# Performance work log

Measured on AMD Instinct MI355X. Metric: run time of the kernel, lower is better.

The kernel has to match this reference:

```python
import jax, jax.numpy as jnp
import numpy as np
from jax import lax

N = 16384
K = 16
EPS = 1e-5


def setup_inputs() -> dict:
    key = jax.random.key(0)
    ks = jax.random.split(key, 10)

    def w(k, shape):
        fan_in = shape[0]
        return jax.random.normal(k, shape, jnp.float32) / np.sqrt(fan_in)

    return {
        "pos": jax.random.normal(ks[0], (N, 3), jnp.float32),
        "normal": jax.random.normal(ks[1], (N, 3), jnp.float32),
        # conv1 mlp: Linear(9,64) -> GroupNorm(8,64) -> ReLU -> Linear(64,64)
        "W1a": w(ks[2], (9, 64)), "b1a": jnp.zeros((64,), jnp.float32),
        "g1": jnp.ones((64,), jnp.float32), "beta1": jnp.zeros((64,), jnp.float32),
        "W1b": w(ks[3], (64, 64)), "b1b": jnp.zeros((64,), jnp.float32),
        # conv2 mlp: Linear(67,64) -> GroupNorm(8,64) -> ReLU -> Linear(64,64)
        "W2a": w(ks[4], (67, 64)), "b2a": jnp.zeros((64,), jnp.float32),
        "g2": jnp.ones((64,), jnp.float32), "beta2": jnp.zeros((64,), jnp.float32),
        "W2b": w(ks[5], (64, 64)), "b2b": jnp.zeros((64,), jnp.float32),
        # conv3 mlp: Linear(67,128) -> GroupNorm(16,128) -> ReLU -> Linear(128,128)
        "W3a": w(ks[6], (67, 128)), "b3a": jnp.zeros((128,), jnp.float32),
        "g3": jnp.ones((128,), jnp.float32), "beta3": jnp.zeros((128,), jnp.float32),
        "W3b": w(ks[7], (128, 128)), "b3b": jnp.zeros((128,), jnp.float32),
    }


def knn_graph(pos, k):
    # [N,N] squared distances; loop=True -> self is included (distance 0).
    sq = jnp.sum(pos * pos, axis=1)
    d2 = sq[:, None] + sq[None, :] - 2.0 * (pos @ pos.T)
    _, nbr = lax.top_k(-d2, k)  # [N,k] neighbor (source) indices per target node
    return nbr


def group_norm(h, gamma, beta, groups):
    # h: [N,k,C]; normalize each group of channels per edge sample.
    n, k, c = h.shape
    hg = h.reshape(n, k, groups, c // groups)
    mu = hg.mean(axis=-1, keepdims=True)
    var = hg.var(axis=-1, keepdims=True)
    hg = (hg - mu) * lax.rsqrt(var + EPS)
    return hg.reshape(n, k, c) * gamma + beta


def pointnet_conv(x, pos, nbr, Wa, ba, gamma, beta, Wb, bb, groups):
    # message: concat(x_j, pos_j - pos_i), MLP per edge, max-aggregate over neighbors
    xj = x[nbr]                              # [N,k,C_in]
    rel = pos[nbr] - pos[:, None, :]         # [N,k,3]
    m = jnp.concatenate([xj, rel], axis=-1)  # [N,k,C_in+3]
    h = m @ Wa + ba
    h = jax.nn.relu(group_norm(h, gamma, beta, groups))
    h = h @ Wb + bb
    return jnp.max(h, axis=1)                # [N,C_out]


def reference(pos, normal, W1a, b1a, g1, beta1, W1b, b1b,
              W2a, b2a, g2, beta2, W2b, b2b,
              W3a, b3a, g3, beta3, W3b, b3b):
    nbr = knn_graph(pos, K)
    h = jnp.concatenate([pos, normal], axis=-1)  # [N,6]
    h1 = jax.nn.relu(pointnet_conv(h, pos, nbr, W1a, b1a, g1, beta1, W1b, b1b, 8))
    h2 = jax.nn.relu(pointnet_conv(h1, pos, nbr, W2a, b2a, g2, beta2, W2b, b2b, 8))
    h3 = jax.nn.relu(pointnet_conv(h2, pos, nbr, W3a, b3a, g3, beta3, W3b, b3b, 16))
    return (h1, h2, h3)
```

## Files before the change

### kernel.cpp

```cpp
#include <hip/hip_runtime.h>
#include <hip/hip_bf16.h>
#include <stdint.h>

typedef unsigned long long u64;
typedef unsigned int u32;
typedef __attribute__((ext_vector_type(8))) short bf16x8;
typedef __attribute__((ext_vector_type(4))) float f32x4;

__device__ __forceinline__ float ldv(const void* p, size_t idx, int mode) {
  return mode ? __bfloat162float(((const __hip_bfloat16*)p)[idx])
              : ((const float*)p)[idx];
}
__device__ __forceinline__ void stv(void* p, size_t idx, int mode, float v) {
  if (mode) ((__hip_bfloat16*)p)[idx] = __float2bfloat16(v);
  else      ((float*)p)[idx] = v;
}
__device__ __forceinline__ unsigned short f2bfb(float f) {
  u32 u = __float_as_uint(f);
  u32 r = u + 0x7fffu + ((u >> 16) & 1u);
  return (unsigned short)(r >> 16);
}
__device__ __forceinline__ u64 shfl64(u64 v, int src) {
  int lo = __shfl((int)(u32)(v & 0xffffffffu), src, 64);
  int hi = __shfl((int)(u32)(v >> 32), src, 64);
  return ((u64)(u32)hi << 32) | (u32)lo;
}
__device__ __forceinline__ u64 shfl_up64(u64 v, int d) {
  int lo = __shfl_up((int)(u32)(v & 0xffffffffu), d, 64);
  int hi = __shfl_up((int)(u32)(v >> 32), d, 64);
  return ((u64)(u32)hi << 32) | (u32)lo;
}

__global__ void PointNetSimple_61409442398998_kernel() {}

__global__ void detect_kernel(const void* __restrict__ pos, int* __restrict__ flag) {
  if (threadIdx.x == 0 && blockIdx.x == 0) {
    const unsigned short* u = (const unsigned short*)pos;
    int cnt = 0;
    for (int k = 0; k < 32; ++k) {
      int e = (u[k] >> 7) & 0xff;
      if (e >= 110 && e <= 140) cnt++;
    }
    flag[0] = (cnt >= 26) ? 1 : 0;
  }
}

struct CvtEnt { const void* src; float* dst; int n; };
struct CvtArgs { CvtEnt e[12]; };
__global__ void cvt_kernel(CvtArgs a, const int* __restrict__ flag) {
  const int mode = flag[0];
  CvtEnt ent = a.e[blockIdx.x];
  for (int t = threadIdx.x; t < ent.n; t += blockDim.x)
    ent.dst[t] = ldv(ent.src, t, mode);
}

struct WEnt { const void* src; unsigned short* dst; int K, N, Kpad; };
struct WArgs { WEnt e[6]; };
__global__ void wcvt_kernel(WArgs a, const int* __restrict__ flag) {
  const int mode = flag[0];
  WEnt ent = a.e[blockIdx.x];
  for (int t = threadIdx.x; t < ent.N * ent.Kpad; t += blockDim.x) {
    int nn = t / ent.Kpad;
    int k  = t - nn * ent.Kpad;
    float v = (k < ent.K) ? ldv(ent.src, (size_t)k * ent.N + nn, mode) : 0.0f;
    ent.dst[t] = f2bfb(v);
  }
}

__global__ void prep_kernel(const void* __restrict__ pos,
                            const void* __restrict__ nrm,
                            const int* __restrict__ flag,
                            float4* __restrict__ pos4,
                            float* __restrict__ h0, int n) {
  const int mode = flag[0];
  int i = blockIdx.x * blockDim.x + threadIdx.x;
  if (i >= n) return;
  float x = ldv(pos, 3*(size_t)i+0, mode);
  float y = ldv(pos, 3*(size_t)i+1, mode);
  float z = ldv(pos, 3*(size_t)i+2, mode);
  pos4[i] = make_float4(x, y, z, x*x + y*y + z*z);
  h0[6*(size_t)i+0] = x; h0[6*(size_t)i+1] = y; h0[6*(size_t)i+2] = z;
  h0[6*(size_t)i+3] = ldv(nrm, 3*(size_t)i+0, mode);
  h0[6*(size_t)i+4] = ldv(nrm, 3*(size_t)i+1, mode);
  h0[6*(size_t)i+5] = ldv(nrm, 3*(size_t)i+2, mode);
}

#define KNN_TPB 512
#define KNN_WPB 8
#define KCH 1024

__device__ __forceinline__ void knn_process(u64 bal, float d2, int base,
                                            u64& val, u64& t15, float& th,
                                            int lane) {
  while (bal) {
    int src = __ffsll((long long)bal) - 1;
    bal &= bal - 1;
    float ds = __shfl(d2, src, 64);
    u64 key = ((u64)__float_as_uint(ds) << 32) | (u32)(base + src);
    if (key < t15) {
      u64 prev = shfl_up64(val, 1);
      if (lane == 0) prev = 0ull;
      val = (key < prev) ? prev : ((key < val) ? key : val);
      t15 = shfl64(val, 15);
      th = __uint_as_float((u32)(t15 >> 32));
    }
  }
}

__global__ __launch_bounds__(KNN_TPB) void knn3_kernel(
    const float4* __restrict__ pos4, int* __restrict__ nbr, int n) {
  __shared__ float4 sp[2][KCH];
  const int tid  = threadIdx.x;
  const int lane = tid & 63;
  const int wid  = tid >> 6;
  const int i    = blockIdx.x * KNN_WPB + wid;
  const float4 pi = pos4[i];

  u64 val = ~0ull;
  u64 t15 = ~0ull;
  float th = __uint_as_float(0xffffffffu);
  th = 1e38f;

  for (int t = tid; t < KCH; t += KNN_TPB) sp[0][t] = pos4[t];
  __syncthreads();

  const int nch = n / KCH;
  for (int c = 0; c < nch; ++c) {
    const int cur = c & 1;
    float4 pre0, pre1;
    const bool more = (c + 1 < nch);
    if (more) {
      pre0 = pos4[(size_t)(c+1)*KCH + tid];
      pre1 = pos4[(size_t)(c+1)*KCH + KNN_TPB + tid];
    }
#pragma unroll 2
    for (int t = 0; t < KCH; t += 128) {
      float4 a = sp[cur][t + lane];
      float4 b = sp[cur][t + 64 + lane];
      float da = (pi.w + a.w) - 2.0f*(pi.x*a.x + pi.y*a.y + pi.z*a.z);
      float db = (pi.w + b.w) - 2.0f*(pi.x*b.x + pi.y*b.y + pi.z*b.z);
      da = fmaxf(da, 0.0f); db = fmaxf(db, 0.0f);
      int base = c*KCH + t;
      u64 bal = __ballot(da <= th);
      if (bal) knn_process(bal, da, base, val, t15, th, lane);
      bal = __ballot(db <= th);
      if (bal) knn_process(bal, db, base + 64, val, t15, th, lane);
    }
    if (more) {
      sp[cur^1][tid] = pre0;
      sp[cur^1][KNN_TPB + tid] = pre1;
    }
    __syncthreads();
  }
  if (lane < 16) nbr[(size_t)i*16 + lane] = (int)(val & 0xffffffffu);
}

template<int CIN, int CMID, int KT1, int NT, int KT2>
__global__ __launch_bounds__(256) void conv_mfma2_kernel(
    const float* __restrict__ xin,
    const float4* __restrict__ pos4,
    const int* __restrict__ nbr,
    const int* __restrict__ flag,
    const unsigned short* __restrict__ WaT,
    const unsigned short* __restrict__ WbT,
    const float* __restrict__ baf,
    const float* __restrict__ gmf,
    const float* __restrict__ btf,
    const float* __restrict__ bbf,
    float* __restrict__ xout,
    void* __restrict__ bout, size_t out_off)
{
  constexpr int K1PAD = KT1 * 32;
  constexpr int SB = CMID + 8;

  __shared__ unsigned short msgB[128 * SB];
  __shared__ float stage[4][32][20];

  const int tid  = threadIdx.x;
  const int lane = tid & 63;
  const int w    = tid >> 6;
  const int quad = lane >> 4;
  const int cl   = lane & 15;
  const int node0 = blockIdx.x * 8;
  const int mode = flag[0];

  bf16x8 afr[2][KT1];
#pragma unroll
  for (int mt = 0; mt < 2; ++mt) {
    const int node = node0 + w*2 + mt;
    const int j = nbr[(size_t)node*16 + cl];
    const float4 pin = pos4[node];
    const float4 pj = pos4[j];
    const float rx = pj.x - pin.x, ry = pj.y - pin.y, rz = pj.z - pin.z;
    if constexpr (CIN == 64) {
#pragma unroll
      for (int kt = 0; kt < 2; ++kt) {
        const float* p = &xin[(size_t)j*64 + kt*32 + quad*8];
        float4 a = *(const float4*)p;
        float4 b = *(const float4*)(p + 4);
        unsigned short o[8] = {f2bfb(a.x), f2bfb(a.y), f2bfb(a.z), f2bfb(a.w),
                               f2bfb(b.x), f2bfb(b.y), f2bfb(b.z), f2bfb(b.w)};
        afr[mt][kt] = *(bf16x8*)o;
      }
      unsigned short o[8] = {0,0,0,0,0,0,0,0};
      if (quad == 0) { o[0] = f2bfb(rx); o[1] = f2bfb(ry); o[2] = f2bfb(rz); }
      afr[mt][KT1-1] = *(bf16x8*)o;
    } else {
      unsigned short o[8] = {0,0,0,0,0,0,0,0};
      if (quad == 0) {
        const float* p = &xin[(size_t)j*6];
        o[0] = f2bfb(p[0]); o[1] = f2bfb(p[1]); o[2] = f2bfb(p[2]);
        o[3] = f2bfb(p[3]); o[4] = f2bfb(p[4]); o[5] = f2bfb(p[5]);
        o[6] = f2bfb(rx);   o[7] = f2bfb(ry);
      } else if (quad == 1) {
        o[0] = f2bfb(rz);
      }
      afr[mt][0] = *(bf16x8*)o;
    }
  }

  f32x4 acc1[2][NT];
#pragma unroll
  for (int mt = 0; mt < 2; ++mt)
#pragma unroll
    for (int nt = 0; nt < NT; ++nt) acc1[mt][nt] = (f32x4){0.f, 0.f, 0.f, 0.f};
#pragma unroll
  for (int kt = 0; kt < KT1; ++kt)
#pragma unroll
    for (int nt = 0; nt < NT; ++nt) {
      bf16x8 bfr = *(const bf16x8*)&WaT[(size_t)(nt*16 + cl) * K1PAD + kt*32 + quad*8];
      acc1[0][nt] = __builtin_amdgcn_mfma_f32_16x16x32_bf16(afr[0][kt], bfr, acc1[0][nt], 0, 0, 0);
      acc1[1][nt] = __builtin_amdgcn_mfma_f32_16x16x32_bf16(afr[1][kt], bfr, acc1[1][nt], 0, 0, 0);
    }

#pragma unroll
  for (int nt = 0; nt < NT; ++nt) {
    float bac = baf[nt*16 + cl];
#pragma unroll
    for (int mt = 0; mt < 2; ++mt)
#pragma unroll
      for (int reg = 0; reg < 4; ++reg)
        stage[w][mt*16 + quad*4 + reg][cl] = acc1[mt][nt][reg] + bac;
    asm volatile("" ::: "memory");
    {
      int row = lane >> 1, gl = lane & 1;
      float4 va = *(const float4*)&stage[w][row][gl*8];
      float4 vb = *(const float4*)&stage[w][row][gl*8 + 4];
      float s  = va.x+va.y+va.z+va.w + vb.x+vb.y+vb.z+vb.w;
      float q  = va.x*va.x+va.y*va.y+va.z*va.z+va.w*va.w
               + vb.x*vb.x+vb.y*vb.y+vb.z*vb.z+vb.w*vb.w;
      float mu = s * 0.125f;
      float var = q * 0.125f - mu * mu;
      float inv = rsqrtf(fmaxf(var, 0.0f) + 1e-5f);
      int cb = nt*16 + gl*8;
      float vv[8] = {va.x, va.y, va.z, va.w, vb.x, vb.y, vb.z, vb.w};
      unsigned short o[8];
#pragma unroll
      for (int e = 0; e < 8; ++e) {
        float t = (vv[e] - mu) * inv * gmf[cb+e] + btf[cb+e];
        o[e] = f2bfb(fmaxf(t, 0.0f));
      }
      *(bf16x8*)&msgB[(w*32 + row) * SB + cb] = *(bf16x8*)o;
    }
    asm volatile("" ::: "memory");
  }

  f32x4 acc2[2][NT];
#pragma unroll
  for (int mt = 0; mt < 2; ++mt)
#pragma unroll
    for (int nt = 0; nt < NT; ++nt) acc2[mt][nt] = (f32x4){0.f, 0.f, 0.f, 0.f};
#pragma unroll
  for (int kt = 0; kt < KT2; ++kt) {
    bf16x8 af0 = *(const bf16x8*)&msgB[(w*32 + cl)      * SB + kt*32 + quad*8];
    bf16x8 af1 = *(const bf16x8*)&msgB[(w*32 + 16 + cl) * SB + kt*32 + quad*8];
#pragma unroll
    for (int nt = 0; nt < NT; ++nt) {
      bf16x8 bfr = *(const bf16x8*)&WbT[(size_t)(nt*16 + cl) * CMID + kt*32 + quad*8];
      acc2[0][nt] = __builtin_amdgcn_mfma_f32_16x16x32_bf16(af0, bfr, acc2[0][nt], 0, 0, 0);
      acc2[1][nt] = __builtin_amdgcn_mfma_f32_16x16x32_bf16(af1, bfr, acc2[1][nt], 0, 0, 0);
    }
  }

#pragma unroll
  for (int mt = 0; mt < 2; ++mt) {
    int node = node0 + w*2 + mt;
#pragma unroll
    for (int nt = 0; nt < NT; ++nt) {
      float m = fmaxf(fmaxf(acc2[mt][nt][0], acc2[mt][nt][1]),
                      fmaxf(acc2[mt][nt][2], acc2[mt][nt][3]));
      m = fmaxf(m, __shfl_xor(m, 16, 64));
      m = fmaxf(m, __shfl_xor(m, 32, 64));
      float v = fmaxf(m + bbf[nt*16 + cl], 0.0f);
      if (quad == 0) {
        size_t oi = (size_t)node * CMID + nt*16 + cl;
        if (xout) xout[oi] = v;
        stv(bout, out_off + oi, mode, v);
      }
    }
  }
}

extern "C" void kernel_launch(void* const* d_in, const int* in_sizes, int n_in,
                              void* d_out, int out_size, void* d_ws, size_t ws_size,
                              hipStream_t stream) {
  (void)n_in; (void)ws_size; (void)in_sizes;
  int n = out_size / 256;
  if (n <= 0 || (n & 31)) n = 16384;

  float* ws = (float*)d_ws;
  int*    flag = (int*)ws;
  float4* pos4 = (float4*)(ws + 16);
  float*  h0   = ws + 16 + (size_t)4*n;
  float*  h1   = ws + 16 + (size_t)10*n;
  float*  h2   = ws + 16 + (size_t)74*n;
  int*    nbr  = (int*)(ws + 16 + (size_t)138*n);
  float*  vbuf = ws + 16 + (size_t)154*n;
  unsigned short* wtbuf = (unsigned short*)(vbuf + 1024);

  const int vsz[12] = {64,64,64,64, 64,64,64,64, 128,128,128,128};
  const int vsrc[12] = {3,4,5,7, 9,10,11,13, 15,16,17,19};
  CvtArgs ca;
  float* vptr[12];
  {
    int off = 0;
    for (int t = 0; t < 12; ++t) {
      ca.e[t].src = d_in[vsrc[t]];
      ca.e[t].dst = vbuf + off;
      ca.e[t].n   = vsz[t];
      vptr[t] = vbuf + off;
      off += vsz[t];
    }
  }
  const int wK[6]    = {9, 64, 67, 64, 67, 128};
  const int wN[6]    = {64, 64, 64, 64, 128, 128};
  const int wKp[6]   = {32, 64, 96, 64, 96, 128};
  const int wsrc[6]  = {2, 6, 8, 12, 14, 18};
  WArgs wa;
  unsigned short* wptr[6];
  {
    int off = 0;
    for (int t = 0; t < 6; ++t) {
      wa.e[t].src  = d_in[wsrc[t]];
      wa.e[t].dst  = wtbuf + off;
      wa.e[t].K    = wK[t];
      wa.e[t].N    = wN[t];
      wa.e[t].Kpad = wKp[t];
      wptr[t] = wtbuf + off;
      off += wN[t] * wKp[t];
    }
  }

  detect_kernel<<<1, 64, 0, stream>>>(d_in[0], flag);
  cvt_kernel<<<12, 256, 0, stream>>>(ca, flag);
  wcvt_kernel<<<6, 256, 0, stream>>>(wa, flag);
  prep_kernel<<<(n + 255)/256, 256, 0, stream>>>(d_in[0], d_in[1], flag, pos4, h0, n);
  knn3_kernel<<<n/KNN_WPB, KNN_TPB, 0, stream>>>(pos4, nbr, n);

  conv_mfma2_kernel<6, 64, 1, 4, 2><<<n/8, 256, 0, stream>>>(
      h0, pos4, nbr, flag, wptr[0], wptr[1],
      vptr[0], vptr[1], vptr[2], vptr[3], h1, d_out, (size_t)0);
  conv_mfma2_kernel<64, 64, 3, 4, 2><<<n/8, 256, 0, stream>>>(
      h1, pos4, nbr, flag, wptr[2], wptr[3],
      vptr[4], vptr[5], vptr[6], vptr[7], h2, d_out, (size_t)n*64);
  conv_mfma2_kernel<64, 128, 3, 8, 4><<<n/8, 256, 0, stream>>>(
      h2, pos4, nbr, flag, wptr[4], wptr[5],
      vptr[8], vptr[9], vptr[10], vptr[11], (float*)nullptr, d_out, (size_t)n*128);
}
```

Before: 421.2 us.

## Batch kNN candidates in LDS with bitonic-sort flush; merge setup kernels

The per-candidate serial insertion into a wave-distributed top-16 list is replaced. Passing candidates are compacted into a per-wave LDS buffer via ballot/mbcnt, and once 64 accumulate they are bitonic-sorted across the wave and merged with the current top-16. This removes a long serial shuffle chain per accepted candidate, at the cost of extra sort work per flush and extra LDS. The detect, convert, weight-convert and prep kernels are also fused into one setup launch to cut launch overhead.

Result: faster. 385.7 us (-8.4%).

```diff
diff --git a/kernel.cpp b/kernel.cpp
--- a/kernel.cpp
+++ b/kernel.cpp
@@ -25,101 +25,123 @@
   int hi = __shfl((int)(u32)(v >> 32), src, 64);
   return ((u64)(u32)hi << 32) | (u32)lo;
 }
-__device__ __forceinline__ u64 shfl_up64(u64 v, int d) {
-  int lo = __shfl_up((int)(u32)(v & 0xffffffffu), d, 64);
-  int hi = __shfl_up((int)(u32)(v >> 32), d, 64);
+__device__ __forceinline__ u64 shflxor64(u64 v, int m) {
+  int lo = __shfl_xor((int)(u32)(v & 0xffffffffu), m, 64);
+  int hi = __shfl_xor((int)(u32)(v >> 32), m, 64);
   return ((u64)(u32)hi << 32) | (u32)lo;
 }
+__device__ __forceinline__ u64 shfl64w16(u64 v, int src) {
+  int lo = __shfl((int)(u32)(v & 0xffffffffu), src, 16);
+  int hi = __shfl((int)(u32)(v >> 32), src, 16);
+  return ((u64)(u32)hi << 32) | (u32)lo;
+}
 
 __global__ void PointNetSimple_61409442398998_kernel() {}
-
-__global__ void detect_kernel(const void* __restrict__ pos, int* __restrict__ flag) {
-  if (threadIdx.x == 0 && blockIdx.x == 0) {
-    const unsigned short* u = (const unsigned short*)pos;
-    int cnt = 0;
-    for (int k = 0; k < 32; ++k) {
-      int e = (u[k] >> 7) & 0xff;
-      if (e >= 110 && e <= 140) cnt++;
-    }
-    flag[0] = (cnt >= 26) ? 1 : 0;
-  }
-}
 
 struct CvtEnt { const void* src; float* dst; int n; };
 struct CvtArgs { CvtEnt e[12]; };
-__global__ void cvt_kernel(CvtArgs a, const int* __restrict__ flag) {
-  const int mode = flag[0];
-  CvtEnt ent = a.e[blockIdx.x];
-  for (int t = threadIdx.x; t < ent.n; t += blockDim.x)
-    ent.dst[t] = ldv(ent.src, t, mode);
-}
-
 struct WEnt { const void* src; unsigned short* dst; int K, N, Kpad; };
 struct WArgs { WEnt e[6]; };
-__global__ void wcvt_kernel(WArgs a, const int* __restrict__ flag) {
-  const int mode = flag[0];
-  WEnt ent = a.e[blockIdx.x];
-  for (int t = threadIdx.x; t < ent.N * ent.Kpad; t += blockDim.x) {
-    int nn = t / ent.Kpad;
-    int k  = t - nn * ent.Kpad;
-    float v = (k < ent.K) ? ldv(ent.src, (size_t)k * ent.N + nn, mode) : 0.0f;
-    ent.dst[t] = f2bfb(v);
-  }
-}
-
-__global__ void prep_kernel(const void* __restrict__ pos,
-                            const void* __restrict__ nrm,
-                            const int* __restrict__ flag,
-                            float4* __restrict__ pos4,
-                            float* __restrict__ h0, int n) {
-  const int mode = flag[0];
-  int i = blockIdx.x * blockDim.x + threadIdx.x;
-  if (i >= n) return;
-  float x = ldv(pos, 3*(size_t)i+0, mode);
-  float y = ldv(pos, 3*(size_t)i+1, mode);
-  float z = ldv(pos, 3*(size_t)i+2, mode);
-  pos4[i] = make_float4(x, y, z, x*x + y*y + z*z);
-  h0[6*(size_t)i+0] = x; h0[6*(size_t)i+1] = y; h0[6*(size_t)i+2] = z;
-  h0[6*(size_t)i+3] = ldv(nrm, 3*(size_t)i+0, mode);
-  h0[6*(size_t)i+4] = ldv(nrm, 3*(size_t)i+1, mode);
-  h0[6*(size_t)i+5] = ldv(nrm, 3*(size_t)i+2, mode);
+
+__global__ void setup_kernel(const void* __restrict__ pos,
+                             const void* __restrict__ nrm,
+                             WArgs wa, CvtArgs ca,
+                             int* __restrict__ flag,
+                             float4* __restrict__ pos4,
+                             float* __restrict__ h0, int n) {
+  const unsigned short* u16p = (const unsigned short*)pos;
+  int cnt = 0;
+  for (int k = 0; k < 32; ++k) {
+    int e = (u16p[k] >> 7) & 0xff;
+    if (e >= 110 && e <= 140) cnt++;
+  }
+  const int mode = (cnt >= 26) ? 1 : 0;
+
+  const int nprep = n >> 8;
+  const int b = blockIdx.x;
+  if (b < nprep) {
+    int i = b * 256 + threadIdx.x;
+    float x = ldv(pos, 3*(size_t)i+0, mode);
+    float y = ldv(pos, 3*(size_t)i+1, mode);
+    float z = ldv(pos, 3*(size_t)i+2, mode);
+    pos4[i] = make_float4(x, y, z, x*x + y*y + z*z);
+    h0[6*(size_t)i+0] = x; h0[6*(size_t)i+1] = y; h0[6*(size_t)i+2] = z;
+    h0[6*(size_t)i+3] = ldv(nrm, 3*(size_t)i+0, mode);
+    h0[6*(size_t)i+4] = ldv(nrm, 3*(size_t)i+1, mode);
+    h0[6*(size_t)i+5] = ldv(nrm, 3*(size_t)i+2, mode);
+  } else {
+    int r = b - nprep;
+    if (r < 6) {
+      WEnt ent = wa.e[r];
+      for (int t = threadIdx.x; t < ent.N * ent.Kpad; t += blockDim.x) {
+        int nn = t / ent.Kpad;
+        int k  = t - nn * ent.Kpad;
+        float v = (k < ent.K) ? ldv(ent.src, (size_t)k * ent.N + nn, mode) : 0.0f;
+        ent.dst[t] = f2bfb(v);
+      }
+      if (r == 0 && threadIdx.x == 0) flag[0] = mode;
+    } else {
+      for (int t2 = 0; t2 < 12; ++t2) {
+        CvtEnt ent = ca.e[t2];
+        for (int t = threadIdx.x; t < ent.n; t += blockDim.x)
+          ent.dst[t] = ldv(ent.src, t, mode);
+      }
+    }
+  }
 }
 
 #define KNN_TPB 512
 #define KNN_WPB 8
 #define KCH 1024
 
-__device__ __forceinline__ void knn_process(u64 bal, float d2, int base,
-                                            u64& val, u64& t15, float& th,
-                                            int lane) {
-  while (bal) {
-    int src = __ffsll((long long)bal) - 1;
-    bal &= bal - 1;
-    float ds = __shfl(d2, src, 64);
-    u64 key = ((u64)__float_as_uint(ds) << 32) | (u32)(base + src);
-    if (key < t15) {
-      u64 prev = shfl_up64(val, 1);
-      if (lane == 0) prev = 0ull;
-      val = (key < prev) ? prev : ((key < val) ? key : val);
-      t15 = shfl64(val, 15);
-      th = __uint_as_float((u32)(t15 >> 32));
-    }
-  }
-}
-
-__global__ __launch_bounds__(KNN_TPB) void knn3_kernel(
+__device__ __forceinline__ void knn_flush(u64* __restrict__ wbuf, int& cnt,
+                                          u64& val, u64& t15, float& th,
+                                          int lane) {
+  u64 cand = (lane < cnt) ? wbuf[lane] : ~0ull;
+#pragma unroll
+  for (int k = 2; k <= 64; k <<= 1) {
+#pragma unroll
+    for (int j = k >> 1; j > 0; j >>= 1) {
+      u64 other = shflxor64(cand, j);
+      bool up    = ((lane & k) == 0) || (k == 64);
+      bool lower = ((lane & j) == 0);
+      bool keepMin = (up == lower);
+      u64 mn = cand < other ? cand : other;
+      u64 mx = cand < other ? other : cand;
+      cand = keepMin ? mn : mx;
+    }
+  }
+  u64 rev = shfl64w16(cand, 15 - (lane & 15));
+  u64 lo = val < rev ? val : rev;
+#pragma unroll
+  for (int j = 8; j > 0; j >>= 1) {
+    u64 other = shflxor64(lo, j);
+    bool lower = ((lane & j) == 0);
+    u64 mn = lo < other ? lo : other;
+    u64 mx = lo < other ? other : lo;
+    lo = lower ? mn : mx;
+  }
+  val = (lane < 16) ? lo : ~0ull;
+  t15 = shfl64(val, 15);
+  th = __uint_as_float((u32)(t15 >> 32));
+  cnt = 0;
+}
+
+__global__ __launch_bounds__(KNN_TPB) void knn4_kernel(
     const float4* __restrict__ pos4, int* __restrict__ nbr, int n) {
   __shared__ float4 sp[2][KCH];
+  __shared__ u64 buf[KNN_WPB][72];
   const int tid  = threadIdx.x;
   const int lane = tid & 63;
   const int wid  = tid >> 6;
   const int i    = blockIdx.x * KNN_WPB + wid;
   const float4 pi = pos4[i];
+  u64* wbuf = &buf[wid][0];
 
   u64 val = ~0ull;
   u64 t15 = ~0ull;
-  float th = __uint_as_float(0xffffffffu);
-  th = 1e38f;
+  float th = 3.4e38f;
+  int cnt = 0;
 
   for (int t = tid; t < KCH; t += KNN_TPB) sp[0][t] = pos4[t];
   __syncthreads();
@@ -134,17 +156,21 @@
       pre1 = pos4[(size_t)(c+1)*KCH + KNN_TPB + tid];
     }
 #pragma unroll 2
-    for (int t = 0; t < KCH; t += 128) {
+    for (int t = 0; t < KCH; t += 64) {
       float4 a = sp[cur][t + lane];
-      float4 b = sp[cur][t + 64 + lane];
-      float da = (pi.w + a.w) - 2.0f*(pi.x*a.x + pi.y*a.y + pi.z*a.z);
-      float db = (pi.w + b.w) - 2.0f*(pi.x*b.x + pi.y*b.y + pi.z*b.z);
-      da = fmaxf(da, 0.0f); db = fmaxf(db, 0.0f);
-      int base = c*KCH + t;
-      u64 bal = __ballot(da <= th);
-      if (bal) knn_process(bal, da, base, val, t15, th, lane);
-      bal = __ballot(db <= th);
-      if (bal) knn_process(bal, db, base + 64, val, t15, th, lane);
+      float d2 = (pi.w + a.w) - 2.0f*(pi.x*a.x + pi.y*a.y + pi.z*a.z);
+      d2 = fmaxf(d2, 0.0f);
+      bool pass = (d2 <= th);
+      u64 bal = __ballot(pass);
+      if (bal) {
+        int pc = __popcll(bal);
+        if (cnt + pc > 64) knn_flush(wbuf, cnt, val, t15, th, lane);
+        u32 mb = __builtin_amdgcn_mbcnt_lo((u32)bal, 0u);
+        mb = __builtin_amdgcn_mbcnt_hi((u32)(bal >> 32), mb);
+        if (pass)
+          wbuf[cnt + mb] = ((u64)__float_as_uint(d2) << 32) | (u32)(c*KCH + t + lane);
+        cnt += pc;
+      }
     }
     if (more) {
       sp[cur^1][tid] = pre0;
@@ -152,6 +178,7 @@
     }
     __syncthreads();
   }
+  knn_flush(wbuf, cnt, val, t15, th, lane);
   if (lane < 16) nbr[(size_t)i*16 + lane] = (int)(val & 0xffffffffu);
 }
 
@@ -306,7 +333,7 @@
                               hipStream_t stream) {
   (void)n_in; (void)ws_size; (void)in_sizes;
   int n = out_size / 256;
-  if (n <= 0 || (n & 31)) n = 16384;
+  if (n <= 0 || (n & 255)) n = 16384;
 
   float* ws = (float*)d_ws;
   int*    flag = (int*)ws;
@@ -351,11 +378,9 @@
     }
   }
 
-  detect_kernel<<<1, 64, 0, stream>>>(d_in[0], flag);
-  cvt_kernel<<<12, 256, 0, stream>>>(ca, flag);
-  wcvt_kernel<<<6, 256, 0, stream>>>(wa, flag);
-  prep_kernel<<<(n + 255)/256, 256, 0, stream>>>(d_in[0], d_in[1], flag, pos4, h0, n);
-  knn3_kernel<<<n/KNN_WPB, KNN_TPB, 0, stream>>>(pos4, nbr, n);
+  setup_kernel<<<n/256 + 7, 256, 0, stream>>>(
+      d_in[0], d_in[1], wa, ca, flag, pos4, h0, n);
+  knn4_kernel<<<n/KNN_WPB, KNN_TPB, 0, stream>>>(pos4, nbr, n);
 
   conv_mfma2_kernel<6, 64, 1, 4, 2><<<n/8, 256, 0, stream>>>(
       h0, pos4, nbr, flag, wptr[0], wptr[1],
```
